# Kernel optimization log

Measured on AMD Instinct MI355X. Metric: run time of the kernel, lower is better.

The kernel has to match this reference:

```python
import jax, jax.numpy as jnp
import numpy as np
import math

B, P, PIX, D, C = 128, 256, 256, 512, 10
MAX_STEPS, TOL, EPS = 4, 1e-3, 1e-5


def setup_inputs() -> dict:
    key = jax.random.key(0)
    ks = jax.random.split(key, 12)
    pi = math.pi
    return {
        "x": jax.random.normal(ks[0], (B, P, PIX), jnp.float32),
        "Wp": jax.random.normal(ks[1], (D, PIX), jnp.float32) * (1.0 / math.sqrt(PIX)),
        "bp": jnp.zeros((D,), jnp.float32),
        "q_rot": jax.random.uniform(ks[2], (D,), jnp.float32, -pi, pi),
        "k_rot": jax.random.uniform(ks[3], (D,), jnp.float32, -pi, pi),
        "v_rot": jax.random.uniform(ks[4], (D,), jnp.float32, -pi, pi),
        "ff_real": jax.random.normal(ks[5], (D, D), jnp.float32) * (1.0 / math.sqrt(D)),
        "ff_imag": jax.random.uniform(ks[6], (D, D), jnp.float32, -0.01, 0.01),
        "Wr": jax.random.normal(ks[7], (C, D), jnp.float32) * 0.05,
        "br": jnp.zeros((C,), jnp.float32),
        "Wi": jax.random.normal(ks[8], (C, D), jnp.float32) * 0.05,
        "bi": jnp.zeros((C,), jnp.float32),
    }


def _complex_norm(x):
    # normalize magnitude stats over last dim, preserve phase (torch.std uses ddof=1)
    mag = jnp.abs(x)
    mean_mag = jnp.mean(mag, axis=-1, keepdims=True)
    std_mag = jnp.std(mag, axis=-1, keepdims=True, ddof=1)
    norm_mag = (mag - mean_mag) / (std_mag + EPS)
    scale = jnp.tanh(norm_mag) / (mag + EPS)
    return x * scale


def _fro(z):
    return jnp.sqrt(jnp.sum(jnp.abs(z) ** 2))


def _pos_phase():
    pos = jnp.arange(P, dtype=jnp.float32)[:, None]
    dim = jnp.arange(D, dtype=jnp.float32)[None, :]
    freq = 1.0 / (10000.0 ** (dim / D))
    return pos * freq * math.pi  # (P, D)


def reference(x, Wp, bp, q_rot, k_rot, v_rot, ff_real, ff_imag, Wr, br, Wi, bi):
    mag = jnp.tanh(jnp.einsum('bpi,di->bpd', x, Wp) + bp)
    state = mag.astype(jnp.complex64) * jnp.exp(1j * _pos_phase())[None]  # (B,P,D)
    ff = (ff_real + 1j * ff_imag).astype(jnp.complex64)
    eq, ek, ev = jnp.exp(1j * q_rot), jnp.exp(1j * k_rot), jnp.exp(1j * v_rot)
    scale = 8.0 / math.sqrt(D)
    active = jnp.array(True)
    for _ in range(MAX_STEPS):  # fixed small iteration count; updates frozen after convergence
        prev = state
        q, k, v = state * eq, state * ek, state * ev
        interference = jnp.einsum('bpd,bqd->bpq', q, jnp.conj(k))
        attn = jax.nn.softmax(interference.real * scale, axis=-1)
        attn_out = jnp.einsum('bpq,bqd->bpd', attn.astype(jnp.complex64), v)
        new_state = _complex_norm((prev + attn_out) @ ff)
        diff = _fro(new_state - prev) / (_fro(new_state) + 1e-8)
        state = jnp.where(active, new_state, prev)
        active = jnp.logical_and(active, diff >= TOL)
    pooled = jnp.mean(state, axis=1)  # (B,D) complex
    logits = pooled.real @ Wr.T + br + pooled.imag @ Wi.T + bi
    return logits
```

## Files before the change

kernel.cpp:

```cpp
#include <hip/hip_runtime.h>
#include <math.h>

#define BB   128
#define PP   256
#define PIX_ 256
#define DD   512
#define CC   10
#define MTOT (BB*PP)
#define NK   1024
#define KA   2048
#define KB2  2048
#define NSLOT (MTOT/4)

static constexpr float SCALE_F = 0.35355339059327373f;
static constexpr float PI_F    = 3.14159265358979323846f;

typedef short bf16x8 __attribute__((ext_vector_type(8)));
typedef float f32x4  __attribute__((ext_vector_type(4)));

__device__ __forceinline__ unsigned short f2bf(float f) {
    union { float f; unsigned u; } v; v.f = f;
    unsigned r = v.u + 0x7FFF + ((v.u >> 16) & 1);
    return (unsigned short)(r >> 16);
}
__device__ __forceinline__ float bf2f(unsigned short h) {
    union { unsigned u; float f; } v; v.u = ((unsigned)h) << 16;
    return v.f;
}

typedef __attribute__((address_space(3))) unsigned lds_u32;
typedef __attribute__((address_space(1))) const unsigned glb_u32;
__device__ __forceinline__ void gl2lds16(const unsigned short* g, short* l) {
    __builtin_amdgcn_global_load_lds((glb_u32*)g, (lds_u32*)l, 16, 0, 0);
}

__global__ void k_setup(const float* __restrict__ q_rot, const float* __restrict__ k_rot,
                        const float* __restrict__ v_rot,
                        float* __restrict__ freq, float* __restrict__ cd, float* __restrict__ sd,
                        float* __restrict__ cv, float* __restrict__ sv,
                        int* __restrict__ active) {
    int t = threadIdx.x;
    if (t < DD) {
        freq[t] = expf(-(float)t * (9.210340371976184f / 512.0f));
        float dl = q_rot[t] - k_rot[t];
        cd[t] = cosf(dl);       sd[t] = sinf(dl);
        cv[t] = cosf(v_rot[t]); sv[t] = sinf(v_rot[t]);
    }
    if (t == 0) *active = 1;
}

__global__ __launch_bounds__(256) void k_prep2(const float* __restrict__ Fr, const float* __restrict__ Fi,
                                               unsigned short* __restrict__ Bt2) {
    const int n = blockIdx.x;
    const int t = threadIdx.x;
    unsigned short* row = Bt2 + (size_t)n * KB2;
#pragma unroll
    for (int j4 = 0; j4 < 4; j4++) {
        const int j = j4 * 256 + t;
        float v;
        if (n < 512) v = (j < 512) ? Fr[(size_t)j * DD + n] : -Fi[(size_t)(j - 512) * DD + n];
        else         v = (j < 512) ? Fi[(size_t)j * DD + (n - 512)] : Fr[(size_t)(j - 512) * DD + (n - 512)];
        const unsigned short hi = f2bf(v);
        row[j] = hi;
        row[NK + j] = f2bf(v - bf2f(hi));
    }
}

#define SCAT4(TILE, V4) do { TILE[lk+0][lrow]=(V4).x; TILE[lk+1][lrow]=(V4).y; \
                             TILE[lk+2][lrow]=(V4).z; TILE[lk+3][lrow]=(V4).w; } while(0)

__global__ __launch_bounds__(256) void k_init(const float* __restrict__ x,
        const float* __restrict__ Wp, const float* __restrict__ bp,
        const float* __restrict__ freq,
        float* __restrict__ Sr, float* __restrict__ Si) {
    __shared__ float As[16][68];
    __shared__ float Bs[16][68];
    const int bm = blockIdx.y * 64, bn = blockIdx.x * 64;
    const int t = threadIdx.x, tx = t & 15, ty = t >> 4;
    const int lrow = t >> 2, lk = (t & 3) * 4;
    float acc[4][4] = {};
    for (int k0 = 0; k0 < PIX_; k0 += 16) {
        const float4 a4 = *(const float4*)(x  + (size_t)(bm + lrow) * PIX_ + k0 + lk);
        const float4 b4 = *(const float4*)(Wp + (size_t)(bn + lrow) * PIX_ + k0 + lk);
        __syncthreads();
        SCAT4(As, a4);
        SCAT4(Bs, b4);
        __syncthreads();
#pragma unroll
        for (int kk = 0; kk < 16; ++kk) {
            const float4 av = *(const float4*)&As[kk][ty * 4];
            const float4 bv = *(const float4*)&Bs[kk][tx * 4];
            const float a[4] = {av.x, av.y, av.z, av.w};
            const float b[4] = {bv.x, bv.y, bv.z, bv.w};
#pragma unroll
            for (int i = 0; i < 4; i++)
#pragma unroll
                for (int j = 0; j < 4; j++) acc[i][j] = fmaf(a[i], b[j], acc[i][j]);
        }
    }
#pragma unroll
    for (int i = 0; i < 4; i++) {
        const int m = bm + ty * 4 + i;
        const int p = m & 255;
        float4 vr, vi;
        float* pvr = (float*)&vr; float* pvi = (float*)&vi;
#pragma unroll
        for (int j = 0; j < 4; j++) {
            const int d = bn + tx * 4 + j;
            const float mg = tanhf(acc[i][j] + bp[d]);
            const float ph = (float)p * freq[d] * PI_F;
            float sph, cph; sincosf(ph, &sph, &cph);
            pvr[j] = mg * cph; pvi[j] = mg * sph;
        }
        *(float4*)(Sr + (size_t)m * DD + bn + tx * 4) = vr;
        *(float4*)(Si + (size_t)m * DD + bn + tx * 4) = vi;
    }
}

__global__ __launch_bounds__(256) void k_xy(const float* __restrict__ Sr, const float* __restrict__ Si,
        const float* __restrict__ cd, const float* __restrict__ sd,
        unsigned short* X, unsigned short* Y,
        const int* __restrict__ active) {
    if (*active == 0) return;
    const int r = blockIdx.x, t = threadIdx.x;
    const size_t base = (size_t)r * DD + 2 * t;
    const float2 s_r = *(const float2*)(Sr + base);
    const float2 s_i = *(const float2*)(Si + base);
    const float2 c2  = *(const float2*)(cd + 2 * t);
    const float2 s2  = *(const float2*)(sd + 2 * t);
    unsigned short* xr = X + (size_t)r * KA;
    unsigned short* yr = Y + (size_t)r * KA;
    const float srv[2] = {s_r.x, s_r.y}, siv[2] = {s_i.x, s_i.y};
    const float cv_[2] = {c2.x, c2.y},  sv_[2] = {s2.x, s2.y};
    ushort2 xh_r, xh_i, xl_r, xl_i, yh_r, yh_i, yl_r, yl_i;
    unsigned short* o[8] = {(unsigned short*)&xh_r, (unsigned short*)&xh_i,
                            (unsigned short*)&xl_r, (unsigned short*)&xl_i,
                            (unsigned short*)&yh_r, (unsigned short*)&yh_i,
                            (unsigned short*)&yl_r, (unsigned short*)&yl_i};
#pragma unroll
    for (int e = 0; e < 2; e++) {
        const unsigned short hr = f2bf(srv[e]);
        const unsigned short hi_ = f2bf(siv[e]);
        o[0][e] = hr;  o[2][e] = f2bf(srv[e] - bf2f(hr));
        o[1][e] = hi_; o[3][e] = f2bf(siv[e] - bf2f(hi_));
        const float krr = srv[e] * cv_[e] + siv[e] * sv_[e];
        const float kri = siv[e] * cv_[e] - srv[e] * sv_[e];
        const unsigned short yh1 = f2bf(krr);
        const unsigned short yh2 = f2bf(kri);
        o[4][e] = yh1; o[6][e] = f2bf(krr - bf2f(yh1));
        o[5][e] = yh2; o[7][e] = f2bf(kri - bf2f(yh2));
    }
    *(ushort2*)(xr + 2 * t)        = xh_r;
    *(ushort2*)(xr + 512 + 2 * t)  = xh_i;
    *(ushort2*)(xr + 1024 + 2 * t) = xl_r;
    *(ushort2*)(xr + 1536 + 2 * t) = xl_i;
    *(ushort2*)(yr + 2 * t)        = yh_r;
    *(ushort2*)(yr + 512 + 2 * t)  = yh_i;
    *(ushort2*)(yr + 1024 + 2 * t) = yl_r;
    *(ushort2*)(yr + 1536 + 2 * t) = yl_i;
}

__global__ __launch_bounds__(256) void k_score_sm(const unsigned short* __restrict__ X,
        const unsigned short* __restrict__ Y,
        unsigned short* __restrict__ Asp, const int* __restrict__ active) {
    if (*active == 0) return;
    __shared__ short XH[64][32], XL[64][32];
    __shared__ short YH[256][32], YL[256][32];
    const int t = threadIdx.x;
    const int w = t >> 6, L = t & 63;
    const int lane15 = L & 15, quad = L >> 4;
    const int nsm = (int)gridDim.x >> 2;
    const int s   = (int)blockIdx.x & (nsm - 1);
    const int rt  = (int)blockIdx.x / nsm;
    const int bm = s * 256 + rt * 64;
    const int yb = s * 256;
    const int gr = t >> 2, ch = (t & 3) * 8;
    short* XHw = &XH[0][0] + w * 512;
    short* XLw = &XL[0][0] + w * 512;
    short* YHw = &YH[0][0] + w * 512;
    short* YLw = &YL[0][0] + w * 512;
    f32x4 acc[16] = {};
    for (int k0 = 0; k0 < 1024; k0 += 32) {
        __syncthreads();
        gl2lds16(X + (size_t)(bm + gr) * KA + k0 + ch,        XHw);
        gl2lds16(X + (size_t)(bm + gr) * KA + 1024 + k0 + ch, XLw);
#pragma unroll
        for (int ss = 0; ss < 4; ss++) {
            gl2lds16(Y + (size_t)(yb + ss * 64 + gr) * KA + k0 + ch,        YHw + ss * 2048);
            gl2lds16(Y + (size_t)(yb + ss * 64 + gr) * KA + 1024 + k0 + ch, YLw + ss * 2048);
        }
        __syncthreads();
        const bf16x8 xh = *(const bf16x8*)&XH[w * 16 + lane15][quad * 8];
        const bf16x8 xl = *(const bf16x8*)&XL[w * 16 + lane15][quad * 8];
#pragma unroll
        for (int tc = 0; tc < 16; tc++) {
            const bf16x8 yh = *(const bf16x8*)&YH[tc * 16 + lane15][quad * 8];
            acc[tc] = __builtin_amdgcn_mfma_f32_16x16x32_bf16(xh, yh, acc[tc], 0, 0, 0);
            acc[tc] = __builtin_amdgcn_mfma_f32_16x16x32_bf16(xl, yh, acc[tc], 0, 0, 0);
            const bf16x8 yl = *(const bf16x8*)&YL[tc * 16 + lane15][quad * 8];
            acc[tc] = __builtin_amdgcn_mfma_f32_16x16x32_bf16(xh, yl, acc[tc], 0, 0, 0);
        }
    }
#pragma unroll
    for (int tc = 0; tc < 16; tc++) acc[tc] *= SCALE_F;
#pragma unroll
    for (int r = 0; r < 4; r++) {
        float mx = acc[0][r];
#pragma unroll
        for (int tc = 1; tc < 16; tc++) mx = fmaxf(mx, acc[tc][r]);
#pragma unroll
        for (int off = 8; off; off >>= 1) mx = fmaxf(mx, __shfl_xor(mx, off, 64));
        float sum = 0.f;
        float e[16];
#pragma unroll
        for (int tc = 0; tc < 16; tc++) { e[tc] = __expf(acc[tc][r] - mx); sum += e[tc]; }
#pragma unroll
        for (int off = 8; off; off >>= 1) sum += __shfl_xor(sum, off, 64);
        const float inv = 1.0f / sum;
        const int row = bm + w * 16 + quad * 4 + r;
        unsigned short* o = Asp + (size_t)row * 512;
#pragma unroll
        for (int tc = 0; tc < 16; tc++) {
            const float p = e[tc] * inv;
            const unsigned short h = f2bf(p);
            o[tc * 16 + lane15] = h;
            o[256 + tc * 16 + lane15] = f2bf(p - bf2f(h));
        }
    }
}

__global__ __launch_bounds__(256) void k_attnout_mfma(const unsigned short* __restrict__ Asp,
        const unsigned short* __restrict__ X,
        const float* __restrict__ Sr, const float* __restrict__ Si,
        const float* __restrict__ cv, const float* __restrict__ sv,
        unsigned short* __restrict__ A2, const int* __restrict__ active) {
    if (*active == 0) return;
    __shared__ short AhT[128][32];
    __shared__ short AlT[128][32];
    __shared__ short BH[128][40];
    __shared__ short BL[128][40];
    const int t = threadIdx.x;
    const int w = t >> 6, L = t & 63;
    const int lane15 = L & 15, quad = L >> 4;
    const int bm = blockIdx.x * 128;
    const int bn = blockIdx.y * 64;
    const int sample = blockIdx.x >> 1;
    const int gr = t >> 2, ch = (t & 3) * 8;
    short* AhW0 = &AhT[0][0] + w * 512;
    short* AhW1 = AhW0 + 64 * 32;
    short* AlW0 = &AlT[0][0] + w * 512;
    short* AlW1 = AlW0 + 64 * 32;
    const int nn = t & 127, kh = t >> 7;
    const unsigned short* Bsrc = X + (size_t)sample * PP * KA
                               + ((nn < 64) ? (bn + nn) : (512 + bn + nn - 64));
    f32x4 acc[2][8] = {};
    for (int q0 = 0; q0 < PP; q0 += 32) {
        __syncthreads();
        gl2lds16(Asp + (size_t)(bm + gr) * 512      + q0 + ch,       AhW0);
        gl2lds16(Asp + (size_t)(bm + 64 + gr) * 512 + q0 + ch,       AhW1);
        gl2lds16(Asp + (size_t)(bm + gr) * 512      + 256 + q0 + ch, AlW0);
        gl2lds16(Asp + (size_t)(bm + 64 + gr) * 512 + 256 + q0 + ch, AlW1);
#pragma unroll
        for (int kg = 0; kg < 2; kg++) {
            const int qb = kh * 16 + kg * 8;
            bf16x8 hh, ll;
#pragma unroll
            for (int j = 0; j < 8; j++) {
                const size_t o = (size_t)(q0 + qb + j) * KA;
                hh[j] = (short)Bsrc[o];
                ll[j] = (short)Bsrc[o + 1024];
            }
            *(bf16x8*)&BH[nn][qb] = hh;
            *(bf16x8*)&BL[nn][qb] = ll;
        }
        __syncthreads();
        bf16x8 bh[8];
#pragma unroll
        for (int tc = 0; tc < 8; tc++)
            bh[tc] = *(const bf16x8*)&BH[tc * 16 + lane15][quad * 8];
        bf16x8 afh[2];
#pragma unroll
        for (int tr = 0; tr < 2; tr++) {
            afh[tr] = *(const bf16x8*)&AhT[w * 32 + tr * 16 + lane15][quad * 8];
            const bf16x8 afl = *(const bf16x8*)&AlT[w * 32 + tr * 16 + lane15][quad * 8];
#pragma unroll
            for (int tc = 0; tc < 8; tc++)
                acc[tr][tc] = __builtin_amdgcn_mfma_f32_16x16x32_bf16(afh[tr], bh[tc], acc[tr][tc], 0, 0, 0);
#pragma unroll
            for (int tc = 0; tc < 8; tc++)
                acc[tr][tc] = __builtin_amdgcn_mfma_f32_16x16x32_bf16(afl, bh[tc], acc[tr][tc], 0, 0, 0);
        }
#pragma unroll
        for (int tc = 0; tc < 8; tc++) {
            const bf16x8 bl = *(const bf16x8*)&BL[tc * 16 + lane15][quad * 8];
            acc[0][tc] = __builtin_amdgcn_mfma_f32_16x16x32_bf16(afh[0], bl, acc[0][tc], 0, 0, 0);
            acc[1][tc] = __builtin_amdgcn_mfma_f32_16x16x32_bf16(afh[1], bl, acc[1][tc], 0, 0, 0);
        }
    }
#pragma unroll
    for (int tr = 0; tr < 2; tr++) {
#pragma unroll
        for (int tc = 0; tc < 4; tc++) {
            const int d = bn + tc * 16 + lane15;
            const float cvd = cv[d], svd = sv[d];
#pragma unroll
            for (int r = 0; r < 4; r++) {
                const int m = bm + w * 32 + tr * 16 + quad * 4 + r;
                const float wr = acc[tr][tc][r];
                const float wi = acc[tr][tc + 4][r];
                const float tr_ = Sr[(size_t)m * DD + d] + (wr * cvd - wi * svd);
                const float ti_ = Si[(size_t)m * DD + d] + (wr * svd + wi * cvd);
                const unsigned short rh = f2bf(tr_);
                const unsigned short ih = f2bf(ti_);
                unsigned short* arow = A2 + (size_t)m * KA;
                arow[d]        = rh;
                arow[512 + d]  = ih;
                arow[1024 + d] = f2bf(tr_ - bf2f(rh));
                arow[1536 + d] = f2bf(ti_ - bf2f(ih));
            }
        }
    }
}

__global__ __launch_bounds__(256) void k_ff_mfma2(const unsigned short* __restrict__ A2,
        const unsigned short* __restrict__ Bt2,
        float* __restrict__ U, const int* __restrict__ active) {
    if (*active == 0) return;
    __shared__ short AH[128][32], AL[128][32];
    __shared__ short BH[128][32], BL[128][32];
    const int t = threadIdx.x;
    const int w = t >> 6, L = t & 63;
    const int lane15 = L & 15, quad = L >> 4;
    const int bm = blockIdx.x * 128, bn = blockIdx.y * 128;
    const int gr = t >> 2, ch = (t & 3) * 8;
    short* AHw = &AH[0][0] + w * 512;
    short* ALw = &AL[0][0] + w * 512;
    short* BHw = &BH[0][0] + w * 512;
    short* BLw = &BL[0][0] + w * 512;
    f32x4 acc[2][8] = {};
    for (int k0 = 0; k0 < 1024; k0 += 32) {
        __syncthreads();
        gl2lds16(A2  + (size_t)(bm + gr) * KA       + k0 + ch,        AHw);
        gl2lds16(A2  + (size_t)(bm + 64 + gr) * KA  + k0 + ch,        AHw + 64 * 32);
        gl2lds16(A2  + (size_t)(bm + gr) * KA       + 1024 + k0 + ch, ALw);
        gl2lds16(A2  + (size_t)(bm + 64 + gr) * KA  + 1024 + k0 + ch, ALw + 64 * 32);
        gl2lds16(Bt2 + (size_t)(bn + gr) * KB2      + k0 + ch,        BHw);
        gl2lds16(Bt2 + (size_t)(bn + 64 + gr) * KB2 + k0 + ch,        BHw + 64 * 32);
        gl2lds16(Bt2 + (size_t)(bn + gr) * KB2      + 1024 + k0 + ch, BLw);
        gl2lds16(Bt2 + (size_t)(bn + 64 + gr) * KB2 + 1024 + k0 + ch, BLw + 64 * 32);
        __syncthreads();
        bf16x8 ah[2], al[2];
#pragma unroll
        for (int tr = 0; tr < 2; tr++) {
            ah[tr] = *(const bf16x8*)&AH[w * 32 + tr * 16 + lane15][quad * 8];
            al[tr] = *(const bf16x8*)&AL[w * 32 + tr * 16 + lane15][quad * 8];
        }
#pragma unroll
        for (int tc = 0; tc < 8; tc++) {
            const bf16x8 bh = *(const bf16x8*)&BH[tc * 16 + lane15][quad * 8];
            acc[0][tc] = __builtin_amdgcn_mfma_f32_16x16x32_bf16(ah[0], bh, acc[0][tc], 0, 0, 0);
            acc[1][tc] = __builtin_amdgcn_mfma_f32_16x16x32_bf16(ah[1], bh, acc[1][tc], 0, 0, 0);
            acc[0][tc] = __builtin_amdgcn_mfma_f32_16x16x32_bf16(al[0], bh, acc[0][tc], 0, 0, 0);
            acc[1][tc] = __builtin_amdgcn_mfma_f32_16x16x32_bf16(al[1], bh, acc[1][tc], 0, 0, 0);
            const bf16x8 bl = *(const bf16x8*)&BL[tc * 16 + lane15][quad * 8];
            acc[0][tc] = __builtin_amdgcn_mfma_f32_16x16x32_bf16(ah[0], bl, acc[0][tc], 0, 0, 0);
            acc[1][tc] = __builtin_amdgcn_mfma_f32_16x16x32_bf16(ah[1], bl, acc[1][tc], 0, 0, 0);
        }
    }
#pragma unroll
    for (int tr = 0; tr < 2; tr++)
#pragma unroll
        for (int tc = 0; tc < 8; tc++) {
            const int n = bn + tc * 16 + lane15;
            const int mbase = bm + w * 32 + tr * 16 + quad * 4;
#pragma unroll
            for (int r = 0; r < 4; r++)
                U[(size_t)(mbase + r) * NK + n] = acc[tr][tc][r];
        }
}

__global__ __launch_bounds__(256) void k_norm(const float* U,
        float* __restrict__ Sr, float* __restrict__ Si,
        float* __restrict__ part,
        unsigned short* X, unsigned short* Y,
        const float* __restrict__ cd, const float* __restrict__ sd,
        const int wxy, const int* __restrict__ active) {
    if (*active == 0) return;
    __shared__ float red[8];
    const int t = threadIdx.x, rt = t >> 6, L = t & 63;
    const int row = blockIdx.x * 4 + rt;
    const size_t ub = (size_t)row * NK;
    const size_t base = (size_t)row * DD;
    const float4 ur0 = *(const float4*)(U + ub + 4 * L);
    const float4 ur1 = *(const float4*)(U + ub + 256 + 4 * L);
    const float4 ui0 = *(const float4*)(U + ub + 512 + 4 * L);
    const float4 ui1 = *(const float4*)(U + ub + 768 + 4 * L);
    const float4 pr0 = *(const float4*)(Sr + base + 4 * L);
    const float4 pr1 = *(const float4*)(Sr + base + 256 + 4 * L);
    const float4 pi0 = *(const float4*)(Si + base + 4 * L);
    const float4 pi1 = *(const float4*)(Si + base + 256 + 4 * L);
    const float urr[8] = {ur0.x, ur0.y, ur0.z, ur0.w, ur1.x, ur1.y, ur1.z, ur1.w};
    const float uii[8] = {ui0.x, ui0.y, ui0.z, ui0.w, ui1.x, ui1.y, ui1.z, ui1.w};
    float mg[8], msum = 0.f;
#pragma unroll
    for (int e = 0; e < 8; e++) {
        mg[e] = sqrtf(urr[e] * urr[e] + uii[e] * uii[e]);
        msum += mg[e];
    }
#pragma unroll
    for (int off = 32; off; off >>= 1) msum += __shfl_xor(msum, off, 64);
    const float mean = msum * (1.0f / 512.0f);
    float vs = 0.f;
#pragma unroll
    for (int e = 0; e < 8; e++) { const float d = mg[e] - mean; vs += d * d; }
#pragma unroll
    for (int off = 32; off; off >>= 1) vs += __shfl_xor(vs, off, 64);
    const float istd = 1.0f / (sqrtf(vs * (1.0f / 511.0f)) + 1e-5f);
    float nr[8], ni[8];
#pragma unroll
    for (int e = 0; e < 8; e++) {
        const float sc = tanhf((mg[e] - mean) * istd) / (mg[e] + 1e-5f);
        nr[e] = urr[e] * sc; ni[e] = uii[e] * sc;
    }
    const float prr[8] = {pr0.x, pr0.y, pr0.z, pr0.w, pr1.x, pr1.y, pr1.z, pr1.w};
    const float pii[8] = {pi0.x, pi0.y, pi0.z, pi0.w, pi1.x, pi1.y, pi1.z, pi1.w};
    float dd = 0.f, nn = 0.f;
#pragma unroll
    for (int e = 0; e < 8; e++) {
        const float dr = nr[e] - prr[e], di = ni[e] - pii[e];
        dd += dr * dr + di * di;
        nn += nr[e] * nr[e] + ni[e] * ni[e];
    }
    *(float4*)(Sr + base + 4 * L)       = make_float4(nr[0], nr[1], nr[2], nr[3]);
    *(float4*)(Sr + base + 256 + 4 * L) = make_float4(nr[4], nr[5], nr[6], nr[7]);
    *(float4*)(Si + base + 4 * L)       = make_float4(ni[0], ni[1], ni[2], ni[3]);
    *(float4*)(Si + base + 256 + 4 * L) = make_float4(ni[4], ni[5], ni[6], ni[7]);
    if (wxy) {
        unsigned short* xr = X + (size_t)row * KA;
        unsigned short* yr = Y + (size_t)row * KA;
        const float4 c0 = *(const float4*)(cd + 4 * L);
        const float4 c1 = *(const float4*)(cd + 256 + 4 * L);
        const float4 s0 = *(const float4*)(sd + 4 * L);
        const float4 s1 = *(const float4*)(sd + 256 + 4 * L);
        const float cdv[8] = {c0.x, c0.y, c0.z, c0.w, c1.x, c1.y, c1.z, c1.w};
        const float sdv[8] = {s0.x, s0.y, s0.z, s0.w, s1.x, s1.y, s1.z, s1.w};
        ushort4 xhr[2], xhi[2], xlr[2], xli[2], yhr[2], yhi[2], ylr[2], yli[2];
#pragma unroll
        for (int e = 0; e < 8; e++) {
            const int g = e >> 2, j = e & 3;
            const unsigned short hr = f2bf(nr[e]);
            const unsigned short hi_ = f2bf(ni[e]);
            ((unsigned short*)&xhr[g])[j] = hr;
            ((unsigned short*)&xlr[g])[j] = f2bf(nr[e] - bf2f(hr));
            ((unsigned short*)&xhi[g])[j] = hi_;
            ((unsigned short*)&xli[g])[j] = f2bf(ni[e] - bf2f(hi_));
            const float krr = nr[e] * cdv[e] + ni[e] * sdv[e];
            const float kri = ni[e] * cdv[e] - nr[e] * sdv[e];
            const unsigned short k1 = f2bf(krr);
            const unsigned short k2 = f2bf(kri);
            ((unsigned short*)&yhr[g])[j] = k1;
            ((unsigned short*)&ylr[g])[j] = f2bf(krr - bf2f(k1));
            ((unsigned short*)&yhi[g])[j] = k2;
            ((unsigned short*)&yli[g])[j] = f2bf(kri - bf2f(k2));
        }
        *(ushort4*)(xr + 4 * L)        = xhr[0]; *(ushort4*)(xr + 256 + 4 * L)  = xhr[1];
        *(ushort4*)(xr + 512 + 4 * L)  = xhi[0]; *(ushort4*)(xr + 768 + 4 * L)  = xhi[1];
        *(ushort4*)(xr + 1024 + 4 * L) = xlr[0]; *(ushort4*)(xr + 1280 + 4 * L) = xlr[1];
        *(ushort4*)(xr + 1536 + 4 * L) = xli[0]; *(ushort4*)(xr + 1792 + 4 * L) = xli[1];
        *(ushort4*)(yr + 4 * L)        = yhr[0]; *(ushort4*)(yr + 256 + 4 * L)  = yhr[1];
        *(ushort4*)(yr + 512 + 4 * L)  = yhi[0]; *(ushort4*)(yr + 768 + 4 * L)  = yhi[1];
        *(ushort4*)(yr + 1024 + 4 * L) = ylr[0]; *(ushort4*)(yr + 1280 + 4 * L) = ylr[1];
        *(ushort4*)(yr + 1536 + 4 * L) = yli[0]; *(ushort4*)(yr + 1792 + 4 * L) = yli[1];
    }
#pragma unroll
    for (int off = 32; off; off >>= 1) {
        dd += __shfl_xor(dd, off, 64);
        nn += __shfl_xor(nn, off, 64);
    }
    if (L == 0) { red[rt] = dd; red[4 + rt] = nn; }
    __syncthreads();
    if (t == 0)
        *(float2*)(part + 2 * blockIdx.x) =
            make_float2(red[0] + red[1] + red[2] + red[3],
                        red[4] + red[5] + red[6] + red[7]);
}

__global__ __launch_bounds__(256) void k_flag(const float* __restrict__ part, int* __restrict__ active) {
    __shared__ float red[8];
    const int t = threadIdx.x, rt = t >> 6, L = t & 63;
    float dd = 0.f, nn = 0.f;
    for (int i = t; i < NSLOT; i += 256) {
        const float2 p = *(const float2*)(part + 2 * i);
        dd += p.x; nn += p.y;
    }
#pragma unroll
    for (int off = 32; off; off >>= 1) {
        dd += __shfl_xor(dd, off, 64);
        nn += __shfl_xor(nn, off, 64);
    }
    if (L == 0) { red[rt] = dd; red[4 + rt] = nn; }
    __syncthreads();
    if (t == 0) {
        const float d = red[0] + red[1] + red[2] + red[3];
        const float n = red[4] + red[5] + red[6] + red[7];
        const float diff = sqrtf(d) / (sqrtf(n) + 1e-8f);
        const int a = *active;
        *active = (a && (diff >= 1e-3f)) ? 1 : 0;
    }
}

__global__ __launch_bounds__(256) void k_pool(const float* __restrict__ Sr, const float* __restrict__ Si,
        float* __restrict__ Pr, float* __restrict__ Pi) {
    const int gid = blockIdx.x * 256 + threadIdx.x;
    const int b = gid >> 9, d = gid & 511;
    const size_t base = (size_t)b * PP * DD + d;
    float sr = 0.f, si = 0.f;
    for (int p = 0; p < PP; p++) {
        sr += Sr[base + (size_t)p * DD];
        si += Si[base + (size_t)p * DD];
    }
    Pr[gid] = sr * (1.0f / 256.0f);
    Pi[gid] = si * (1.0f / 256.0f);
}

__global__ __launch_bounds__(64) void k_logits(const float* __restrict__ Pr, const float* __restrict__ Pi,
        const float* __restrict__ Wr, const float* __restrict__ br,
        const float* __restrict__ Wi, const float* __restrict__ bi,
        float* __restrict__ out) {
    const int b = blockIdx.x;
    const int lane = threadIdx.x;
    for (int c = 0; c < CC; c++) {
        float acc = 0.f;
#pragma unroll
        for (int k = 0; k < 8; k++) {
            const int d = lane + 64 * k;
            acc += Pr[b * DD + d] * Wr[c * DD + d] + Pi[b * DD + d] * Wi[c * DD + d];
        }
#pragma unroll
        for (int off = 32; off; off >>= 1) acc += __shfl_xor(acc, off, 64);
        if (lane == 0) out[b * CC + c] = acc + br[c] + bi[c];
    }
}

extern "C" void kernel_launch(void* const* d_in, const int* in_sizes, int n_in,
                              void* d_out, int out_size, void* d_ws, size_t ws_size,
                              hipStream_t stream) {
    const float* x     = (const float*)d_in[0];
    const float* Wp    = (const float*)d_in[1];
    const float* bp    = (const float*)d_in[2];
    const float* q_rot = (const float*)d_in[3];
    const float* k_rot = (const float*)d_in[4];
    const float* v_rot = (const float*)d_in[5];
    const float* ffr   = (const float*)d_in[6];
    const float* ffi   = (const float*)d_in[7];
    const float* Wr    = (const float*)d_in[8];
    const float* br    = (const float*)d_in[9];
    const float* Wi    = (const float*)d_in[10];
    const float* bi    = (const float*)d_in[11];
    float* out = (float*)d_out;

    float* ws = (float*)d_ws;
    const size_t plane = (size_t)MTOT * DD;
    const size_t sline = (size_t)PP * DD;

    float* freq = ws;
    float* cd   = freq + DD;
    float* sd   = cd + DD;
    float* cv   = sd + DD;
    float* sv   = cv + DD;
    int*   active = (int*)(sv + DD);
    float* Pr = ws + 4096;
    float* Pi = Pr + (size_t)BB * DD;
    float* part = Pi + (size_t)BB * DD;
    float* Sr = part + 2 * NSLOT;
    float* Si = Sr + plane;
    unsigned short* Bt2 = (unsigned short*)(Si + plane);
    float* chunkbase = Si + plane + (size_t)NK * 3072 / 2;

    const size_t fixed_f = (4096 + 2 * (size_t)BB * DD + 2 * NSLOT) + 2 * plane + (size_t)NK * 3072 / 2;
    const size_t perC_f = (size_t)PP * NK * 2 + (size_t)PP * 256;

    int C = BB;
    while (C > 1 && (fixed_f + (size_t)C * perC_f) * 4ull > ws_size) C >>= 1;
    const int fullXY = (C == BB);

    float* U = chunkbase;
    unsigned short* X  = (unsigned short*)chunkbase;
    float* Yf = chunkbase + (size_t)C * PP * NK;
    unsigned short* Y  = (unsigned short*)Yf;
    unsigned short* A2 = Y;
    unsigned short* Asp = (unsigned short*)(Yf + (size_t)C * PP * NK);

    k_setup<<<1, 512, 0, stream>>>(q_rot, k_rot, v_rot, freq, cd, sd, cv, sv, active);
    k_prep2<<<NK, 256, 0, stream>>>(ffr, ffi, Bt2);
    k_init<<<dim3(DD / 64, MTOT / 64), 256, 0, stream>>>(x, Wp, bp, freq, Sr, Si);

    for (int it = 0; it < 4; ++it) {
        for (int c0 = 0; c0 < BB; c0 += C) {
            float* Sr_c = Sr + (size_t)c0 * sline;
            float* Si_c = Si + (size_t)c0 * sline;
            float* part_c = part + (size_t)c0 * (PP / 4) * 2;
            if (!fullXY || it == 0)
                k_xy<<<C * PP, 256, 0, stream>>>(Sr_c, Si_c, cd, sd, X, Y, active);
            k_score_sm<<<C * 4, 256, 0, stream>>>(X, Y, Asp, active);
            k_attnout_mfma<<<dim3(C * 2, 8), 256, 0, stream>>>(Asp, X, Sr_c, Si_c, cv, sv, A2, active);
            k_ff_mfma2<<<dim3(C * 2, NK / 128), 256, 0, stream>>>(A2, Bt2, U, active);
            k_norm<<<C * (PP / 4), 256, 0, stream>>>(U, Sr_c, Si_c, part_c, X, Y, cd, sd, fullXY, active);
        }
        k_flag<<<1, 256, 0, stream>>>(part, active);
    }

    k_pool<<<BB * DD / 256, 256, 0, stream>>>(Sr, Si, Pr, Pi);
    k_logits<<<BB, 64, 0, stream>>>(Pr, Pi, Wr, br, Wi, bi, out);
}
```

Before: 3.008 ms.

## Stage softmax output through LDS for coalesced stores; precompute positional sincos table

```diff
diff --git a/kernel.cpp b/kernel.cpp
--- a/kernel.cpp
+++ b/kernel.cpp
@@ -17,6 +17,7 @@
 
 typedef short bf16x8 __attribute__((ext_vector_type(8)));
 typedef float f32x4  __attribute__((ext_vector_type(4)));
+typedef unsigned short ushort8 __attribute__((ext_vector_type(8)));
 
 __device__ __forceinline__ unsigned short f2bf(float f) {
     union { float f; unsigned u; } v; v.f = f;
@@ -49,6 +50,18 @@
     if (t == 0) *active = 1;
 }
 
+__global__ __launch_bounds__(256) void k_tab(const float* __restrict__ freq,
+                                             float* __restrict__ Tc, float* __restrict__ Ts) {
+    const int p = blockIdx.x, t = threadIdx.x;
+#pragma unroll
+    for (int j = 0; j < 2; j++) {
+        const int d = t * 2 + j;
+        float s, c; sincosf((float)p * freq[d] * PI_F, &s, &c);
+        Tc[(size_t)p * DD + d] = c;
+        Ts[(size_t)p * DD + d] = s;
+    }
+}
+
 __global__ __launch_bounds__(256) void k_prep2(const float* __restrict__ Fr, const float* __restrict__ Fi,
                                                unsigned short* __restrict__ Bt2) {
     const int n = blockIdx.x;
@@ -71,7 +84,7 @@
 
 __global__ __launch_bounds__(256) void k_init(const float* __restrict__ x,
         const float* __restrict__ Wp, const float* __restrict__ bp,
-        const float* __restrict__ freq,
+        const float* __restrict__ Tc, const float* __restrict__ Ts,
         float* __restrict__ Sr, float* __restrict__ Si) {
     __shared__ float As[16][68];
     __shared__ float Bs[16][68];
@@ -102,15 +115,17 @@
     for (int i = 0; i < 4; i++) {
         const int m = bm + ty * 4 + i;
         const int p = m & 255;
+        const float4 c4 = *(const float4*)(Tc + (size_t)p * DD + bn + tx * 4);
+        const float4 s4 = *(const float4*)(Ts + (size_t)p * DD + bn + tx * 4);
+        const float cphv[4] = {c4.x, c4.y, c4.z, c4.w};
+        const float sphv[4] = {s4.x, s4.y, s4.z, s4.w};
         float4 vr, vi;
         float* pvr = (float*)&vr; float* pvi = (float*)&vi;
 #pragma unroll
         for (int j = 0; j < 4; j++) {
             const int d = bn + tx * 4 + j;
             const float mg = tanhf(acc[i][j] + bp[d]);
-            const float ph = (float)p * freq[d] * PI_F;
-            float sph, cph; sincosf(ph, &sph, &cph);
-            pvr[j] = mg * cph; pvi[j] = mg * sph;
+            pvr[j] = mg * cphv[j]; pvi[j] = mg * sphv[j];
         }
         *(float4*)(Sr + (size_t)m * DD + bn + tx * 4) = vr;
         *(float4*)(Si + (size_t)m * DD + bn + tx * 4) = vi;
@@ -164,8 +179,11 @@
         const unsigned short* __restrict__ Y,
         unsigned short* __restrict__ Asp, const int* __restrict__ active) {
     if (*active == 0) return;
-    __shared__ short XH[64][32], XL[64][32];
-    __shared__ short YH[256][32], YL[256][32];
+    __shared__ short SM[20480];
+    short* XH = SM;
+    short* XL = SM + 2048;
+    short* YH = SM + 4096;
+    short* YL = SM + 12288;
     const int t = threadIdx.x;
     const int w = t >> 6, L = t & 63;
     const int lane15 = L & 15, quad = L >> 4;
@@ -175,10 +193,10 @@
     const int bm = s * 256 + rt * 64;
     const int yb = s * 256;
     const int gr = t >> 2, ch = (t & 3) * 8;
-    short* XHw = &XH[0][0] + w * 512;
-    short* XLw = &XL[0][0] + w * 512;
-    short* YHw = &YH[0][0] + w * 512;
-    short* YLw = &YL[0][0] + w * 512;
+    short* XHw = XH + w * 512;
+    short* XLw = XL + w * 512;
+    short* YHw = YH + w * 512;
+    short* YLw = YL + w * 512;
     f32x4 acc[16] = {};
     for (int k0 = 0; k0 < 1024; k0 += 32) {
         __syncthreads();
@@ -190,14 +208,14 @@
             gl2lds16(Y + (size_t)(yb + ss * 64 + gr) * KA + 1024 + k0 + ch, YLw + ss * 2048);
         }
         __syncthreads();
-        const bf16x8 xh = *(const bf16x8*)&XH[w * 16 + lane15][quad * 8];
-        const bf16x8 xl = *(const bf16x8*)&XL[w * 16 + lane15][quad * 8];
+        const bf16x8 xh = *(const bf16x8*)(XH + (w * 16 + lane15) * 32 + quad * 8);
+        const bf16x8 xl = *(const bf16x8*)(XL + (w * 16 + lane15) * 32 + quad * 8);
 #pragma unroll
         for (int tc = 0; tc < 16; tc++) {
-            const bf16x8 yh = *(const bf16x8*)&YH[tc * 16 + lane15][quad * 8];
+            const bf16x8 yh = *(const bf16x8*)(YH + (tc * 16 + lane15) * 32 + quad * 8);
             acc[tc] = __builtin_amdgcn_mfma_f32_16x16x32_bf16(xh, yh, acc[tc], 0, 0, 0);
             acc[tc] = __builtin_amdgcn_mfma_f32_16x16x32_bf16(xl, yh, acc[tc], 0, 0, 0);
-            const bf16x8 yl = *(const bf16x8*)&YL[tc * 16 + lane15][quad * 8];
+            const bf16x8 yl = *(const bf16x8*)(YL + (tc * 16 + lane15) * 32 + quad * 8);
             acc[tc] = __builtin_amdgcn_mfma_f32_16x16x32_bf16(xh, yl, acc[tc], 0, 0, 0);
         }
     }
@@ -211,21 +229,39 @@
 #pragma unroll
         for (int off = 8; off; off >>= 1) mx = fmaxf(mx, __shfl_xor(mx, off, 64));
         float sum = 0.f;
-        float e[16];
-#pragma unroll
-        for (int tc = 0; tc < 16; tc++) { e[tc] = __expf(acc[tc][r] - mx); sum += e[tc]; }
+#pragma unroll
+        for (int tc = 0; tc < 16; tc++) { acc[tc][r] = __expf(acc[tc][r] - mx); sum += acc[tc][r]; }
 #pragma unroll
         for (int off = 8; off; off >>= 1) sum += __shfl_xor(sum, off, 64);
         const float inv = 1.0f / sum;
-        const int row = bm + w * 16 + quad * 4 + r;
-        unsigned short* o = Asp + (size_t)row * 512;
-#pragma unroll
-        for (int tc = 0; tc < 16; tc++) {
-            const float p = e[tc] * inv;
-            const unsigned short h = f2bf(p);
-            o[tc * 16 + lane15] = h;
-            o[256 + tc * 16 + lane15] = f2bf(p - bf2f(h));
-        }
+#pragma unroll
+        for (int tc = 0; tc < 16; tc++) acc[tc][r] *= inv;
+    }
+    __syncthreads();
+#pragma unroll
+    for (int h = 0; h < 2; h++) {
+        if ((w >> 1) == h) {
+#pragma unroll
+            for (int r = 0; r < 4; r++) {
+                const int lr = (w & 1) * 16 + quad * 4 + r;
+#pragma unroll
+                for (int tc = 0; tc < 16; tc++) {
+                    const float p = acc[tc][r];
+                    const unsigned short hi = f2bf(p);
+                    SM[lr * 520 + tc * 16 + lane15] = (short)hi;
+                    SM[lr * 520 + 256 + tc * 16 + lane15] = (short)f2bf(p - bf2f(hi));
+                }
+            }
+        }
+        __syncthreads();
+        unsigned short* dst = Asp + (size_t)(bm + h * 32) * 512;
+#pragma unroll
+        for (int k = 0; k < 8; k++) {
+            const int c = t + 256 * k;
+            const int row = c >> 6, off = (c & 63) * 8;
+            *(ushort8*)(dst + (size_t)c * 8) = *(const ushort8*)&SM[row * 520 + off];
+        }
+        __syncthreads();
     }
 }
 
@@ -575,6 +611,8 @@
     float* Sr = part + 2 * NSLOT;
     float* Si = Sr + plane;
     unsigned short* Bt2 = (unsigned short*)(Si + plane);
+    float* Tc = (float*)(Bt2 + (size_t)NK * KB2);
+    float* Ts = Tc + (size_t)PP * DD;
     float* chunkbase = Si + plane + (size_t)NK * 3072 / 2;
 
     const size_t fixed_f = (4096 + 2 * (size_t)BB * DD + 2 * NSLOT) + 2 * plane + (size_t)NK * 3072 / 2;
@@ -592,8 +630,9 @@
     unsigned short* Asp = (unsigned short*)(Yf + (size_t)C * PP * NK);
 
     k_setup<<<1, 512, 0, stream>>>(q_rot, k_rot, v_rot, freq, cd, sd, cv, sv, active);
+    k_tab<<<PP, 256, 0, stream>>>(freq, Tc, Ts);
     k_prep2<<<NK, 256, 0, stream>>>(ffr, ffi, Bt2);
-    k_init<<<dim3(DD / 64, MTOT / 64), 256, 0, stream>>>(x, Wp, bp, freq, Sr, Si);
+    k_init<<<dim3(DD / 64, MTOT / 64), 256, 0, stream>>>(x, Wp, bp, Tc, Ts, Sr, Si);
 
     for (int it = 0; it < 4; ++it) {
         for (int c0 = 0; c0 < BB; c0 += C) {
```

New measurement: 3.003 ms. About the same (-0.2%).
